# Kernel optimization log

Hardware: AMD Instinct MI355X
Metric: run time of the kernel (lower is better)

Reference implementation:

```python
import jax, jax.numpy as jnp
import numpy as np

N_NODES = 50000
N_EDGES = 1600000
N_FEAT = 256
HIDDEN = 32
N_CLASS = 64
PROP_RANGE = 4
ALPHA = 0.5
BETA = 1.0


def _spmm(edge_src, edge_dst, edge_val, X):
    # sparse propMatrix @ X : gather source rows, scale by edge weight, scatter-add to dst
    msgs = X[edge_src] * edge_val[:, None]            # [E, C]
    return jax.ops.segment_sum(msgs, edge_dst, num_segments=N_NODES)  # [N, C]


def setup_inputs() -> dict:
    key = jax.random.key(0)
    ks = jax.random.split(key, 8)
    x = jax.random.normal(ks[0], (N_NODES, N_FEAT), dtype=jnp.float32)
    edge_src = jax.random.randint(ks[1], (N_EDGES,), 0, N_NODES, dtype=jnp.int32)
    edge_dst = jax.random.randint(ks[2], (N_EDGES,), 0, N_NODES, dtype=jnp.int32)
    edge_val = jax.random.uniform(ks[3], (N_EDGES,), dtype=jnp.float32)
    # predSeq params: Linear(nFeature,32) -> ReLU -> Linear(32,nClass)
    W1 = jax.random.normal(ks[4], (N_FEAT, HIDDEN), dtype=jnp.float32) / np.sqrt(N_FEAT)
    b1 = jnp.zeros((HIDDEN,), dtype=jnp.float32)
    W2 = jax.random.normal(ks[5], (HIDDEN, N_CLASS), dtype=jnp.float32) / np.sqrt(HIDDEN)
    b2 = jnp.zeros((N_CLASS,), dtype=jnp.float32)
    return {"x": x, "edge_src": edge_src, "edge_dst": edge_dst, "edge_val": edge_val,
            "W1": W1, "b1": b1, "W2": W2, "b2": b2}


def reference(x, edge_src, edge_dst, edge_val, W1, b1, W2, b2):
    # predSeq + softmax -> initial pseudo labels [N, nClass]
    h = jax.nn.relu(x @ W1 + b1)
    p = jax.nn.softmax(h @ W2 + b2, axis=1)
    # prop(), mode='none': propRange steps of nonlinear SpMM (dropout = identity in eval)
    for _ in range(PROP_RANGE):
        p = ALPHA * jnp.tanh(BETA * _spmm(edge_src, edge_dst, edge_val, p))
    return jax.nn.softmax(p, axis=1)
```

## Files before the change

kernel.cpp:

```cpp
#include <hip/hip_runtime.h>
#include <hip/hip_bf16.h>
#include <math.h>

#define N_NODES 50000
#define N_EDGES 1600000
#define N_FEAT  256
#define HIDDEN  32
#define N_CLASS 64
#define NBUCK   391
#define EPB     2560
#define BINB    625
#define MLPB    782
#define SCAP    5120
#define CAP     4608

typedef _Float16 half_t;
typedef _Float16 half8 __attribute__((ext_vector_type(8)));

__device__ __forceinline__ float half_tanh(float x) {
  float e = __expf(2.f * x);
  return 0.5f - __builtin_amdgcn_rcpf(e + 1.f);
}


__global__ __launch_bounds__(256) void prep_kernel(
    const float* __restrict__ x, const float* __restrict__ W1,
    const float* __restrict__ b1, const float* __restrict__ W2,
    const float* __restrict__ b2, half_t* __restrict__ P,
    const int* __restrict__ esrc, const int* __restrict__ edst,
    const float* __restrict__ evl, int* __restrict__ bcur,
    int2* __restrict__ st) {
  __shared__ __align__(16) int smem[6684];
  int t = threadIdx.x;

  if (blockIdx.x >= BINB) {
    float* fs = (float*)smem;
    float* xs = fs;
    float* ps = fs;
    float* hfull = fs + 4416;
    int w = __builtin_amdgcn_readfirstlane(t >> 6);
    int l = t & 63;
    int n0 = (blockIdx.x - BINB) * 64;
    int rowb = t >> 4, c4 = t & 15;
    int f0 = c4 * 4;

    float4 v[4];
#pragma unroll
    for (int p = 0; p < 4; ++p) {
      int row = rowb + 16 * p;
      v[p] = make_float4(0.f, 0.f, 0.f, 0.f);
      if (n0 + row < N_NODES)
        v[p] = *(const float4*)(x + (size_t)(n0 + row) * N_FEAT + f0);
    }

    float h[8];
#pragma unroll
    for (int j = 0; j < 8; ++j) h[j] = 0.f;

    for (int kc = 0; kc < 4; ++kc) {
#pragma unroll
      for (int p = 0; p < 4; ++p) {
        int row = rowb + 16 * p;
        int col = (row + f0) & 63;
        xs[(f0 + 0) * 64 + col] = v[p].x;
        xs[(f0 + 1) * 64 + col] = v[p].y;
        xs[(f0 + 2) * 64 + col] = v[p].z;
        xs[(f0 + 3) * 64 + col] = v[p].w;
      }
      __syncthreads();
      if (kc < 3) {
#pragma unroll
        for (int p = 0; p < 4; ++p) {
          int row = rowb + 16 * p;
          v[p] = make_float4(0.f, 0.f, 0.f, 0.f);
          if (n0 + row < N_NODES)
            v[p] = *(const float4*)(x + (size_t)(n0 + row) * N_FEAT + (kc + 1) * 64 + f0);
        }
      }
#pragma unroll 8
      for (int k = 0; k < 64; ++k) {
        float xk = xs[k * 64 + ((l + (k & 60)) & 63)];
        const float* wr = W1 + (size_t)(kc * 64 + k) * HIDDEN + 8 * w;
#pragma unroll
        for (int j = 0; j < 8; ++j) h[j] = fmaf(xk, wr[j], h[j]);
      }
      __syncthreads();
    }

#pragma unroll
    for (int i = 0; i < 8; ++i)
      hfull[l * 33 + 8 * w + i] = fmaxf(h[i] + b1[8 * w + i], 0.f);
    __syncthreads();

    float pa[16];
#pragma unroll
    for (int c = 0; c < 16; ++c) pa[c] = b2[16 * w + c];
#pragma unroll 4
    for (int kk = 0; kk < 32; ++kk) {
      float hk = hfull[l * 33 + kk];
      const float* w2r = W2 + kk * N_CLASS + 16 * w;
#pragma unroll
      for (int c = 0; c < 16; ++c) pa[c] = fmaf(hk, w2r[c], pa[c]);
    }
#pragma unroll
    for (int c = 0; c < 16; ++c) ps[l * 65 + 16 * w + c] = pa[c];
    __syncthreads();

    {
      int n = t >> 2, ck = (t & 3) * 16;
      float q[16];
      float m = -1e30f;
#pragma unroll
      for (int i = 0; i < 16; ++i) { q[i] = ps[n * 65 + ck + i]; m = fmaxf(m, q[i]); }
      m = fmaxf(m, __shfl_xor(m, 1));
      m = fmaxf(m, __shfl_xor(m, 2));
      float s = 0.f;
#pragma unroll
      for (int i = 0; i < 16; ++i) { q[i] = __expf(q[i] - m); s += q[i]; }
      s += __shfl_xor(s, 1);
      s += __shfl_xor(s, 2);
      float inv = 1.f / s;
      if (n0 + n < N_NODES) {
        half8 o0, o1;
#pragma unroll
        for (int i = 0; i < 8; ++i) {
          o0[i] = (half_t)(q[i] * inv);
          o1[i] = (half_t)(q[8 + i] * inv);
        }
        half_t* op = P + (size_t)(n0 + n) * N_CLASS + ck;
        *(half8*)op = o0;
        *(half8*)(op + 8) = o1;
      }
    }
  } else {
    int2* stage = (int2*)smem;
    int* h      = smem + 5120;
    int* lstart = smem + 5511;
    int* lcur   = smem + 5902;
    int* gbase  = smem + 6293;
    int bb = blockIdx.x;
    for (int i = t; i < NBUCK; i += 256) { h[i] = 0; lcur[i] = 0; }
    __syncthreads();
    int base = bb * EPB;
    int nloc = min(EPB, N_EDGES - base);
    for (int i = t; i < nloc; i += 256) atomicAdd(&h[edst[base + i] >> 7], 1);
    __syncthreads();
    if (t < 64) {
      int loc[7];
      int s0 = 0;
#pragma unroll
      for (int i = 0; i < 7; ++i) {
        int b = t * 7 + i;
        int c = (b < NBUCK) ? h[b] : 0;
        loc[i] = s0; s0 += c;
      }
      int run = s0;
#pragma unroll
      for (int off = 1; off < 64; off <<= 1) {
        int u = __shfl_up(run, off);
        if (t >= off) run += u;
      }
      int excl = run - s0;
#pragma unroll
      for (int i = 0; i < 7; ++i) {
        int b = t * 7 + i;
        if (b < NBUCK) lstart[b] = excl + loc[i];
      }
    }
    __syncthreads();
    for (int i = t; i < NBUCK; i += 256) {
      int c = h[i];
      gbase[i] = c ? atomicAdd(&bcur[i], c) : 0;
    }
    __syncthreads();
    for (int i = t; i < nloc; i += 256) {
      int e = base + i;
      int d = edst[e];
      int b = d >> 7;
      int pos = lstart[b] + atomicAdd(&lcur[b], 1);
      stage[pos] = make_int2((d << 16) | esrc[e], __float_as_int(evl[e]));
    }
    __syncthreads();
    for (int i = t; i < nloc; i += 256) {
      int2 vv = stage[i];
      int b = (int)(((unsigned)vv.x) >> 23);
      int pos = gbase[b] + (i - lstart[b]);
      if (pos < SCAP) st[(size_t)b * SCAP + pos] = vv;
    }
  }
}


__global__ __launch_bounds__(1024) void build_csr(const int* __restrict__ bcur,
                                                  const int2* __restrict__ st,
                                                  int2* __restrict__ rr,
                                                  int2* __restrict__ ep) {
  __shared__ int2 stage[CAP];
  __shared__ int lh[128], lstart[128], lcur[128];
  int b = blockIdx.x, t = threadIdx.x;
  int n = min(min(bcur[b], SCAP), CAP);
  int gb = b * SCAP;
  if (t < 128) { lh[t] = 0; lcur[t] = 0; }
  __syncthreads();
  for (int i = t; i < n; i += 1024) {
    int2 v = st[gb + i];
    stage[i] = v;
    atomicAdd(&lh[(v.x >> 16) & 127], 1);
  }
  __syncthreads();
  if (t < 64) {
    int a0 = lh[2 * t], a1 = lh[2 * t + 1];
    int s0 = a0 + a1;
    int run = s0;
#pragma unroll
    for (int off = 1; off < 64; off <<= 1) {
      int u = __shfl_up(run, off);
      if (t >= off) run += u;
    }
    int excl = run - s0;
    lstart[2 * t] = excl;
    lstart[2 * t + 1] = excl + a0;
  }
  __syncthreads();
  int nodebase = b * 128;
  int nn = min(128, N_NODES - nodebase);
  if (t < nn)
    rr[nodebase + t] = make_int2(gb + lstart[t], gb + lstart[t] + lh[t]);
  for (int i = t; i < n; i += 1024) {
    int2 v = stage[i];
    int d = (v.x >> 16) & 127;
    int pos = lstart[d] + atomicAdd(&lcur[d], 1);
    ep[gb + pos] = make_int2(v.x & 0xffff, v.y);
  }
}


template <int FINAL>
__global__ __launch_bounds__(256) void spmm_kernel(const int2* __restrict__ rr,
                                                   const long long* __restrict__ epl,
                                                   const half_t* __restrict__ pin,
                                                   void* __restrict__ pout_) {
  int tid = threadIdx.x;
  int lane = tid & 63;
  int hf = lane >> 5;
  int sl = lane & 31;
  int g = sl >> 3;
  int s = lane & 7;
  int node = blockIdx.x * 8 + (tid >> 6) * 2 + hf;
  int2 be = rr[node];
  int beg = be.x, end = be.y;
  float acc[8];
#pragma unroll
  for (int i = 0; i < 8; ++i) acc[i] = 0.f;
  for (int base = beg; base < end; base += 32) {
    int idx = base + sl;
    long long raw = (idx < end) ? epl[idx] : 0LL;
    int ex = (int)raw;
    float ev = __int_as_float((int)(raw >> 32));
    int cnt = min(32, end - base);
#pragma unroll 4
    for (int j = g; j < cnt; j += 4) {
      int srcl = (hf << 5) + j;
      int   sj = __shfl(ex, srcl);
      float vj = __shfl(ev, srcl);
      half8 hv = *(const half8*)(pin + ((size_t)sj << 6) + (s << 3));
#pragma unroll
      for (int i = 0; i < 8; ++i) acc[i] = fmaf(vj, (float)hv[i], acc[i]);
    }
  }
#pragma unroll
  for (int off = 8; off <= 16; off <<= 1)
#pragma unroll
    for (int i = 0; i < 8; ++i) acc[i] += __shfl_xor(acc[i], off);
  float r[8];
#pragma unroll
  for (int i = 0; i < 8; ++i) r[i] = half_tanh(acc[i]);
  if (FINAL) {
    float m = r[0];
#pragma unroll
    for (int i = 1; i < 8; ++i) m = fmaxf(m, r[i]);
    m = fmaxf(m, __shfl_xor(m, 1));
    m = fmaxf(m, __shfl_xor(m, 2));
    m = fmaxf(m, __shfl_xor(m, 4));
    float e[8], sum = 0.f;
#pragma unroll
    for (int i = 0; i < 8; ++i) { e[i] = __expf(r[i] - m); sum += e[i]; }
    sum += __shfl_xor(sum, 1);
    sum += __shfl_xor(sum, 2);
    sum += __shfl_xor(sum, 4);
    float inv = 1.f / sum;
    if (g == 0) {
      float* op = (float*)pout_ + ((size_t)node << 6) + (s << 3);
      *(float4*)op = make_float4(e[0] * inv, e[1] * inv, e[2] * inv, e[3] * inv);
      *(float4*)(op + 4) = make_float4(e[4] * inv, e[5] * inv, e[6] * inv, e[7] * inv);
    }
  } else {
    if (g == 0) {
      half8 o;
#pragma unroll
      for (int i = 0; i < 8; ++i) o[i] = (half_t)r[i];
      *(half8*)((half_t*)pout_ + ((size_t)node << 6) + (s << 3)) = o;
    }
  }
}


extern "C" void kernel_launch(void* const* d_in, const int* in_sizes, int n_in,
                              void* d_out, int out_size, void* d_ws, size_t ws_size,
                              hipStream_t stream) {
  const float* x    = (const float*)d_in[0];
  const int*   esrc = (const int*)d_in[1];
  const int*   edst = (const int*)d_in[2];
  const float* evl  = (const float*)d_in[3];
  const float* W1   = (const float*)d_in[4];
  const float* b1   = (const float*)d_in[5];
  const float* W2   = (const float*)d_in[6];
  const float* b2   = (const float*)d_in[7];

  char* ws = (char*)d_ws;
  int2*   st   = (int2*)  (ws);
  half_t* Pb   = (half_t*)(ws);
  int2*   ep   = (int2*)  (ws + 16015360);
  half_t* Pa   = (half_t*)(ws + 32030720);
  int*    bcur = (int*)   (ws + 38430720);
  int2*   rr   = (int2*)  (ws + 38432320);

  hipMemsetAsync(bcur, 0, NBUCK * sizeof(int), stream);

  prep_kernel<<<MLPB + BINB, 256, 0, stream>>>(x, W1, b1, W2, b2, Pa,
                                               esrc, edst, evl, bcur, st);
  build_csr<<<NBUCK, 1024, 0, stream>>>(bcur, st, rr, ep);

  const long long* epl = (const long long*)ep;
  spmm_kernel<0><<<6250, 256, 0, stream>>>(rr, epl, Pa, (void*)Pb);
  spmm_kernel<0><<<6250, 256, 0, stream>>>(rr, epl, Pb, (void*)Pa);
  spmm_kernel<0><<<6250, 256, 0, stream>>>(rr, epl, Pa, (void*)Pb);
  spmm_kernel<1><<<6250, 256, 0, stream>>>(rr, epl, Pb, d_out);
}
```

Before: 260.2 us.

## Pack CSR edges into 32-bit words and batch the first 64 edge gathers

Each edge is now stored as one 32-bit word: a 16-bit source index in the low half and the edge weight as fp16 in the high half. This halves the edge-array traffic read by each of the four SpMM passes and removes one shuffle per edge. The first 32 edges, and the next 32 when degree exceeds 32, are processed in fully unrolled batches of eight independent row gathers to raise memory-level parallelism. The trade-offs are lower weight precision from fp16 rounding and some wasted zero-weight gathers for low-degree nodes.

Result: faster. 239.2 us (-8.1%).

```diff
diff --git a/kernel.cpp b/kernel.cpp
--- a/kernel.cpp
+++ b/kernel.cpp
@@ -194,7 +194,7 @@
 __global__ __launch_bounds__(1024) void build_csr(const int* __restrict__ bcur,
                                                   const int2* __restrict__ st,
                                                   int2* __restrict__ rr,
-                                                  int2* __restrict__ ep) {
+                                                  unsigned* __restrict__ ep4) {
   __shared__ int2 stage[CAP];
   __shared__ int lh[128], lstart[128], lcur[128];
   int b = blockIdx.x, t = threadIdx.x;
@@ -230,14 +230,16 @@
     int2 v = stage[i];
     int d = (v.x >> 16) & 127;
     int pos = lstart[d] + atomicAdd(&lcur[d], 1);
-    ep[gb + pos] = make_int2(v.x & 0xffff, v.y);
+    unsigned uh = (unsigned)__builtin_bit_cast(unsigned short,
+                                               (_Float16)__int_as_float(v.y));
+    ep4[gb + pos] = (unsigned)(v.x & 0xffff) | (uh << 16);
   }
 }
 
 
 template <int FINAL>
 __global__ __launch_bounds__(256) void spmm_kernel(const int2* __restrict__ rr,
-                                                   const long long* __restrict__ epl,
+                                                   const unsigned* __restrict__ ep4,
                                                    const half_t* __restrict__ pin,
                                                    void* __restrict__ pout_) {
   int tid = threadIdx.x;
@@ -247,27 +249,61 @@
   int g = sl >> 3;
   int s = lane & 7;
   int node = blockIdx.x * 8 + (tid >> 6) * 2 + hf;
+  int srcb = hf << 5;
   int2 be = rr[node];
   int beg = be.x, end = be.y;
+  int deg = end - beg;
   float acc[8];
 #pragma unroll
   for (int i = 0; i < 8; ++i) acc[i] = 0.f;
-  for (int base = beg; base < end; base += 32) {
-    int idx = base + sl;
-    long long raw = (idx < end) ? epl[idx] : 0LL;
-    int ex = (int)raw;
-    float ev = __int_as_float((int)(raw >> 32));
-    int cnt = min(32, end - base);
+
+  unsigned raw0 = (sl < deg) ? ep4[beg + sl] : 0u;
+  unsigned raw1 = (sl + 32 < deg) ? ep4[beg + sl + 32] : 0u;
+
+  {
+    float vjs[8];
+    half8 hvv[8];
+#pragma unroll
+    for (int jj = 0; jj < 8; ++jj) {
+      unsigned wj = (unsigned)__shfl((int)raw0, srcb + g + 4 * jj);
+      vjs[jj] = (float)__builtin_bit_cast(_Float16, (unsigned short)(wj >> 16));
+      hvv[jj] = *(const half8*)(pin + ((size_t)(wj & 0xffffu) << 6) + (s << 3));
+    }
+#pragma unroll
+    for (int jj = 0; jj < 8; ++jj)
+#pragma unroll
+      for (int i = 0; i < 8; ++i)
+        acc[i] = fmaf(vjs[jj], (float)hvv[jj][i], acc[i]);
+  }
+  if (deg > 32) {
+    float vjs[8];
+    half8 hvv[8];
+#pragma unroll
+    for (int jj = 0; jj < 8; ++jj) {
+      unsigned wj = (unsigned)__shfl((int)raw1, srcb + g + 4 * jj);
+      vjs[jj] = (float)__builtin_bit_cast(_Float16, (unsigned short)(wj >> 16));
+      hvv[jj] = *(const half8*)(pin + ((size_t)(wj & 0xffffu) << 6) + (s << 3));
+    }
+#pragma unroll
+    for (int jj = 0; jj < 8; ++jj)
+#pragma unroll
+      for (int i = 0; i < 8; ++i)
+        acc[i] = fmaf(vjs[jj], (float)hvv[jj][i], acc[i]);
+    for (int base = beg + 64; base < end; base += 32) {
+      int idx = base + sl;
+      unsigned raw = (idx < end) ? ep4[idx] : 0u;
+      int cnt = min(32, end - base);
 #pragma unroll 4
-    for (int j = g; j < cnt; j += 4) {
-      int srcl = (hf << 5) + j;
-      int   sj = __shfl(ex, srcl);
-      float vj = __shfl(ev, srcl);
-      half8 hv = *(const half8*)(pin + ((size_t)sj << 6) + (s << 3));
-#pragma unroll
-      for (int i = 0; i < 8; ++i) acc[i] = fmaf(vj, (float)hv[i], acc[i]);
-    }
-  }
+      for (int j = g; j < cnt; j += 4) {
+        unsigned wj = (unsigned)__shfl((int)raw, srcb + j);
+        float vj = (float)__builtin_bit_cast(_Float16, (unsigned short)(wj >> 16));
+        half8 hv = *(const half8*)(pin + ((size_t)(wj & 0xffffu) << 6) + (s << 3));
+#pragma unroll
+        for (int i = 0; i < 8; ++i) acc[i] = fmaf(vj, (float)hv[i], acc[i]);
+      }
+    }
+  }
+
 #pragma unroll
   for (int off = 8; off <= 16; off <<= 1)
 #pragma unroll
@@ -318,22 +354,21 @@
   const float* b2   = (const float*)d_in[7];
 
   char* ws = (char*)d_ws;
-  int2*   st   = (int2*)  (ws);
-  half_t* Pb   = (half_t*)(ws);
-  int2*   ep   = (int2*)  (ws + 16015360);
-  half_t* Pa   = (half_t*)(ws + 32030720);
-  int*    bcur = (int*)   (ws + 38430720);
-  int2*   rr   = (int2*)  (ws + 38432320);
+  int2*     st   = (int2*)    (ws);
+  half_t*   Pb   = (half_t*)  (ws);
+  unsigned* ep4  = (unsigned*)(ws + 16015360);
+  half_t*   Pa   = (half_t*)  (ws + 24023040);
+  int*      bcur = (int*)     (ws + 30423040);
+  int2*     rr   = (int2*)    (ws + 30424640);
 
   hipMemsetAsync(bcur, 0, NBUCK * sizeof(int), stream);
 
   prep_kernel<<<MLPB + BINB, 256, 0, stream>>>(x, W1, b1, W2, b2, Pa,
                                                esrc, edst, evl, bcur, st);
-  build_csr<<<NBUCK, 1024, 0, stream>>>(bcur, st, rr, ep);
-
-  const long long* epl = (const long long*)ep;
-  spmm_kernel<0><<<6250, 256, 0, stream>>>(rr, epl, Pa, (void*)Pb);
-  spmm_kernel<0><<<6250, 256, 0, stream>>>(rr, epl, Pb, (void*)Pa);
-  spmm_kernel<0><<<6250, 256, 0, stream>>>(rr, epl, Pa, (void*)Pb);
-  spmm_kernel<1><<<6250, 256, 0, stream>>>(rr, epl, Pb, d_out);
-}
+  build_csr<<<NBUCK, 1024, 0, stream>>>(bcur, st, rr, ep4);
+
+  spmm_kernel<0><<<6250, 256, 0, stream>>>(rr, ep4, Pa, (void*)Pb);
+  spmm_kernel<0><<<6250, 256, 0, stream>>>(rr, ep4, Pb, (void*)Pa);
+  spmm_kernel<0><<<6250, 256, 0, stream>>>(rr, ep4, Pa, (void*)Pb);
+  spmm_kernel<1><<<6250, 256, 0, stream>>>(rr, ep4, Pb, d_out);
+}
```
